# Kernel tuning notes

Hardware: AMD Instinct MI355X
Metric: run time of the kernel (lower is better)

The kernel has to match this reference:

```python
import jax, jax.numpy as jnp
import numpy as np

B, S, D = 2, 2048, 1024
H, HD = 16, 64          # num_heads, head_dim = dim_feedforward // num_heads
ROPE_BASE = 10000.0


def _apply_rope(t):
    # t: [b, h, s, hd] -> RoPE applied over last dim, positions = token index
    b, h, s, hd = t.shape
    theta = 1.0 / (ROPE_BASE ** (jnp.arange(0, hd, 2, dtype=jnp.float32) / hd))  # [hd/2]
    ang = jnp.arange(s, dtype=jnp.float32)[:, None] * theta[None, :]             # [s, hd/2]
    cos, sin = jnp.cos(ang), jnp.sin(ang)
    tr = t.reshape(b, h, s, hd // 2, 2)
    t0, t1 = tr[..., 0], tr[..., 1]
    o0 = t0 * cos - t1 * sin
    o1 = t1 * cos + t0 * sin
    return jnp.stack([o0, o1], axis=-1).reshape(b, h, s, hd)


def setup_inputs() -> dict:
    key = jax.random.key(0)
    ks = jax.random.split(key, 8)
    x = jax.random.normal(ks[0], (B, S, D), dtype=jnp.float32)
    wq = jax.random.normal(ks[1], (D, H * HD), dtype=jnp.float32) * 0.02
    wk = jax.random.normal(ks[2], (D, H * HD), dtype=jnp.float32) * 0.02
    wv = jax.random.normal(ks[3], (D, H * HD), dtype=jnp.float32) * 0.02
    bq = jax.random.normal(ks[4], (H * HD,), dtype=jnp.float32) * 0.02
    bk = jax.random.normal(ks[5], (H * HD,), dtype=jnp.float32) * 0.02
    bv = jax.random.normal(ks[6], (H * HD,), dtype=jnp.float32) * 0.02
    # trailing padding per batch; valid_len large enough that every causal+history
    # window contains at least one unpadded key (valid_len > S - max_history)
    valid_len = jax.random.randint(ks[7], (B,), S - 256, S + 1)
    key_padding_mask = (jnp.arange(S)[None, :] >= valid_len[:, None]).astype(jnp.int32)
    return {"x": x, "wq": wq, "bq": bq, "wk": wk, "bk": bk, "wv": wv, "bv": bv,
            "key_padding_mask": key_padding_mask, "max_history_len": 512}


def reference(x, wq, bq, wk, bk, wv, bv, key_padding_mask, max_history_len):
    b, s, d = x.shape
    scale = HD ** (-0.5)
    q = (x @ wq + bq).reshape(b, s, H, HD).transpose(0, 2, 1, 3)  # [b,h,s,hd]
    k = (x @ wk + bk).reshape(b, s, H, HD).transpose(0, 2, 1, 3)
    v = (x @ wv + bv).reshape(b, s, H, HD).transpose(0, 2, 1, 3)
    q = _apply_rope(q)
    k = _apply_rope(k)
    scores = jnp.einsum('bhqd,bhkd->bhqk', q, k) * scale          # [b,h,s,s]
    i = jnp.arange(s)[:, None]
    j = jnp.arange(s)[None, :]
    band = (j <= i) & ((i - j) <= (max_history_len - 1))          # causal + history
    allowed = band[None, None, :, :] & (key_padding_mask == 0)[:, None, None, :]
    scores = jnp.where(allowed, scores, -jnp.inf)
    attn = jax.nn.softmax(scores, axis=-1)
    out = jnp.einsum('bhqk,bhkd->bhqd', attn, v)                  # [b,h,s,hd]
    return out.transpose(0, 2, 1, 3).reshape(b, s, H * HD)
```

## Files before the change

kernel.cpp:

```cpp
#include <hip/hip_runtime.h>
#include <hip/hip_bf16.h>
#include <stdint.h>


typedef __attribute__((ext_vector_type(8))) short bf16x8;
typedef __attribute__((ext_vector_type(4))) short bf16x4;
typedef __attribute__((ext_vector_type(4))) float f32x4;

#define DEV __device__ __forceinline__

DEV ushort f2b(float f) {
  union { float f; uint32_t u; } v; v.f = f;
  uint32_t r = v.u + 0x7FFFu + ((v.u >> 16) & 1u);
  return (ushort)(r >> 16);
}
DEV float b2f(ushort u) {
  union { uint32_t u; float f; } v; v.u = ((uint32_t)u) << 16;
  return v.f;
}
DEV uint cvt_pk_bf16(float lo, float hi) {
  uint r;
  asm("v_cvt_pk_bf16_f32 %0, %1, %2" : "=v"(r) : "v"(lo), "v"(hi));
  return r;
}
DEV float fast_exp2(float x) {
#if __has_builtin(__builtin_amdgcn_exp2f)
  return __builtin_amdgcn_exp2f(x);
#else
  return exp2f(x);
#endif
}

DEV void gload_lds16(const void* g, void* l) {
  __builtin_amdgcn_global_load_lds((const __attribute__((address_space(1))) void*)g,
                                   (__attribute__((address_space(3))) void*)l,
                                   16, 0, 0);
}

__global__ __launch_bounds__(256) void prep_kernel(
    const float* __restrict__ x, ushort* __restrict__ xb,
    const float* __restrict__ wq, const float* __restrict__ wk,
    const float* __restrict__ wv, ushort* __restrict__ wt,
    float2* __restrict__ tab) {
  int bid = blockIdx.x, tid = threadIdx.x;
  if (bid < 4096) {
    int t = bid * 256 + tid;
    float4 v = ((const float4*)x)[t];
    bf16x4 o;
    o[0] = (short)f2b(v.x); o[1] = (short)f2b(v.y);
    o[2] = (short)f2b(v.z); o[3] = (short)f2b(v.w);
    *(bf16x4*)&xb[(size_t)t * 4] = o;
  } else if (bid < 4352) {
    int t = (bid - 4096) * 256 + tid;
    int i = t & 31, s = t >> 5;
    float theta = powf(10000.0f, -(float)i / 32.0f);
    float ang = (float)s * theta;
    tab[t] = make_float2(cosf(ang), sinf(ang));
  } else {
    __shared__ float tile[32][33];
    int rem = bid - 4352;
    int which = rem >> 10, t2 = rem & 1023;
    int n0 = (t2 & 31) * 32, k0 = (t2 >> 5) * 32;
    const float* w = which == 0 ? wq : (which == 1 ? wk : wv);
    int r = tid >> 3, c4 = (tid & 7) * 4;
    float4 v = *(const float4*)&w[(size_t)(k0 + r) * 1024 + n0 + c4];
    tile[r][c4] = v.x; tile[r][c4 + 1] = v.y;
    tile[r][c4 + 2] = v.z; tile[r][c4 + 3] = v.w;
    __syncthreads();
    bf16x4 o;
#pragma unroll
    for (int i = 0; i < 4; ++i) o[i] = (short)f2b(tile[c4 + i][r]);
    *(bf16x4*)&wt[((size_t)(which * 1024 + n0 + r)) * 1024 + k0 + c4] = o;
  }
}

__global__ __launch_bounds__(512, 2) void qkv_gemm_kernel(
    const ushort* __restrict__ A, const ushort* __restrict__ Bt,
    const float* __restrict__ bq, const float* __restrict__ bk,
    const float* __restrict__ bv, const float2* __restrict__ tab,
    ushort* __restrict__ qb, ushort* __restrict__ kb, ushort* __restrict__ vt) {
  const int K = 1024;
  __shared__ alignas(16) ushort sA[2][256 * 64];
  __shared__ alignas(16) ushort sB[2][192 * 64];

  int tid = threadIdx.x;
  int lane = tid & 63;
  int lhi = lane >> 4, llo = lane & 15;
  int wid = tid >> 6;
  int wr = wid >> 2, wc = wid & 3;

  int id = blockIdx.x;
  int wg = (id & 7) * 32 + (id >> 3);
  int bm = wg >> 4, bn = wg & 15;

  const ushort* Abase = A + (size_t)bm * 256 * K;
  const ushort* Bbase = Bt + (size_t)bn * 192 * K;

  f32x4 acc[8][3];
#pragma unroll
  for (int i = 0; i < 8; ++i)
#pragma unroll
    for (int j = 0; j < 3; ++j) acc[i][j] = (f32x4){0.f, 0.f, 0.f, 0.f};

  auto stage = [&](int kt, int bb) {
    int k0 = kt * 64;
#pragma unroll
    for (int c = 0; c < 4; ++c) {
      int idx = c * 512 + tid;
      int row = idx >> 3, gslot = (idx & 7) ^ (row & 7);
      gload_lds16(Abase + (size_t)row * K + k0 + gslot * 8, &sA[bb][(idx & ~63) * 8]);
    }
#pragma unroll
    for (int c = 0; c < 3; ++c) {
      int idx = c * 512 + tid;
      int row = idx >> 3, gslot = (idx & 7) ^ (row & 7);
      gload_lds16(Bbase + (size_t)row * K + k0 + gslot * 8, &sB[bb][(idx & ~63) * 8]);
    }
  };

  bf16x8 bfr[3][2], af0[4][2], af1[4][2];

  auto readG0 = [&](const ushort* pA, const ushort* pB) {
#pragma unroll
    for (int nf = 0; nf < 3; ++nf) {
      int r = wc * 48 + nf * 16 + llo;
#pragma unroll
      for (int ks = 0; ks < 2; ++ks)
        bfr[nf][ks] = *(const bf16x8*)&pB[r * 64 + (((ks * 4 + lhi) ^ (r & 7)) * 8)];
    }
#pragma unroll
    for (int mf = 0; mf < 4; ++mf) {
      int r = wr * 128 + mf * 16 + llo;
#pragma unroll
      for (int ks = 0; ks < 2; ++ks)
        af0[mf][ks] = *(const bf16x8*)&pA[r * 64 + (((ks * 4 + lhi) ^ (r & 7)) * 8)];
    }
  };
  auto readG1 = [&](const ushort* pA) {
#pragma unroll
    for (int mf = 0; mf < 4; ++mf) {
      int r = wr * 128 + (4 + mf) * 16 + llo;
#pragma unroll
      for (int ks = 0; ks < 2; ++ks)
        af1[mf][ks] = *(const bf16x8*)&pA[r * 64 + (((ks * 4 + lhi) ^ (r & 7)) * 8)];
    }
  };

  stage(0, 0); stage(1, 1);
  asm volatile("s_waitcnt vmcnt(7)" ::: "memory");
  __builtin_amdgcn_sched_barrier(0);
  __builtin_amdgcn_s_barrier();
  __builtin_amdgcn_sched_barrier(0);
  readG0(sA[0], sB[0]);

  for (int kt = 0; kt < 16; ++kt) {
    int buf = kt & 1;
    readG1(sA[buf]);
    asm volatile("s_waitcnt lgkmcnt(8)" ::: "memory");
    __builtin_amdgcn_sched_barrier(0);
    __builtin_amdgcn_s_setprio(1);
#pragma unroll
    for (int mf = 0; mf < 4; ++mf)
#pragma unroll
      for (int nf = 0; nf < 3; ++nf)
#pragma unroll
        for (int ks = 0; ks < 2; ++ks)
          acc[mf][nf] = __builtin_amdgcn_mfma_f32_16x16x32_bf16(bfr[nf][ks], af0[mf][ks], acc[mf][nf], 0, 0, 0);
    __builtin_amdgcn_s_setprio(0);
    asm volatile("s_waitcnt lgkmcnt(0)" ::: "memory");
    __builtin_amdgcn_sched_barrier(0);
    __builtin_amdgcn_s_setprio(1);
#pragma unroll
    for (int mf = 0; mf < 4; ++mf)
#pragma unroll
      for (int nf = 0; nf < 3; ++nf)
#pragma unroll
        for (int ks = 0; ks < 2; ++ks)
          acc[4 + mf][nf] = __builtin_amdgcn_mfma_f32_16x16x32_bf16(bfr[nf][ks], af1[mf][ks], acc[4 + mf][nf], 0, 0, 0);
    __builtin_amdgcn_s_setprio(0);
    __builtin_amdgcn_sched_barrier(0);
    __builtin_amdgcn_s_barrier();
    __builtin_amdgcn_sched_barrier(0);
    if (kt + 2 < 16) stage(kt + 2, buf);
    if (kt + 1 < 16) {
      if (kt + 2 < 16) asm volatile("s_waitcnt vmcnt(7)" ::: "memory");
      else             asm volatile("s_waitcnt vmcnt(0)" ::: "memory");
      __builtin_amdgcn_sched_barrier(0);
      __builtin_amdgcn_s_barrier();
      __builtin_amdgcn_sched_barrier(0);
      readG0(sA[buf ^ 1], sB[buf ^ 1]);
    }
  }

  const float SCL = 0.18033688011112042f;
#pragma unroll
  for (int mf = 0; mf < 8; ++mf) {
    int m = bm * 256 + wr * 128 + mf * 16 + llo;
    int s = m & 2047, bidx = m >> 11;
#pragma unroll
    for (int nf = 0; nf < 3; ++nf) {
      int nbase = bn * 192 + wc * 48 + nf * 16;
      int n0 = nbase + lhi * 4;
      f32x4 a = acc[mf][nf];
      if (nbase < 1024) {
        float4 cs = *(const float4*)&tab[s * 32 + ((n0 & 63) >> 1)];
        float4 bb = *(const float4*)&bq[n0];
        float t0 = a[0] + bb.x, t1 = a[1] + bb.y;
        float t2 = a[2] + bb.z, t3 = a[3] + bb.w;
        uint2 ov;
        ov.x = cvt_pk_bf16((t0 * cs.x - t1 * cs.y) * SCL, (t1 * cs.x + t0 * cs.y) * SCL);
        ov.y = cvt_pk_bf16((t2 * cs.z - t3 * cs.w) * SCL, (t3 * cs.z + t2 * cs.w) * SCL);
        int h = n0 >> 6;
        *(uint2*)&qb[((size_t)(bidx * 16 + h) * 2048 + s) * 64 + (n0 & 63)] = ov;
      } else if (nbase < 2048) {
        float4 cs = *(const float4*)&tab[s * 32 + ((n0 & 63) >> 1)];
        float4 bb = *(const float4*)&bk[n0 - 1024];
        float t0 = a[0] + bb.x, t1 = a[1] + bb.y;
        float t2 = a[2] + bb.z, t3 = a[3] + bb.w;
        uint2 ov;
        ov.x = cvt_pk_bf16(t0 * cs.x - t1 * cs.y, t1 * cs.x + t0 * cs.y);
        ov.y = cvt_pk_bf16(t2 * cs.z - t3 * cs.w, t3 * cs.z + t2 * cs.w);
        int h = (n0 >> 6) & 15;
        *(uint2*)&kb[((size_t)(bidx * 16 + h) * 2048 + s) * 64 + (n0 & 63)] = ov;
      } else {
        float4 bb = *(const float4*)&bv[n0 - 2048];
        int hd_g = n0 - 2048;
        int h = hd_g >> 6, hd = hd_g & 63;
        size_t vb = ((size_t)(bidx * 16 + h) * 64 + hd) * 2048 + s;
        vt[vb]        = f2b(a[0] + bb.x);
        vt[vb + 2048] = f2b(a[1] + bb.y);
        vt[vb + 4096] = f2b(a[2] + bb.z);
        vt[vb + 6144] = f2b(a[3] + bb.w);
      }
    }
  }
}

__global__ __launch_bounds__(512) void attn_kernel(
    const ushort* __restrict__ qb, const ushort* __restrict__ kb,
    const ushort* __restrict__ vt, const int* __restrict__ kmask,
    const int* __restrict__ whist, float* __restrict__ out) {
  __shared__ alignas(16) ushort sK[128 * 64];
  __shared__ alignas(16) ushort sV[64 * 136];
  __shared__ alignas(16) uint   sPd[8][16 * 68];

  int tid = threadIdx.x;
  int lane = tid & 63, wid = tid >> 6;
  int lhi = lane >> 4, llo = lane & 15;

  int id = blockIdx.x;
  int xcd = id & 7, sub = id >> 3;
  int bh = xcd * 4 + (sub >> 4);
  int qtile = sub & 15;
  int b = bh >> 4;
  int q0 = qtile * 128;
  int qw0 = q0 + wid * 16;
  int W = *whist;

  const ushort* qptr = qb + (size_t)bh * 2048 * 64;
  const ushort* kptr = kb + (size_t)bh * 2048 * 64;
  const ushort* vptr = vt + (size_t)bh * 64 * 2048;
  const int* mrow = kmask + b * 2048;

  bf16x8 qf0, qf1;
  {
    size_t base = (size_t)(qw0 + llo) * 64 + lhi * 8;
    qf0 = *(const bf16x8*)&qptr[base];
    qf1 = *(const bf16x8*)&qptr[base + 32];
  }

  float l_ = 0.f;
  f32x4 o[4];
#pragma unroll
  for (int nf = 0; nf < 4; ++nf) o[nf] = (f32x4){0.f, 0.f, 0.f, 0.f};

  int lo = q0 - (W - 1); if (lo < 0) lo = 0;
  int jt0 = lo & ~127;
  int nt = ((q0 + 128) - jt0) >> 7;

  bf16x8 kreg[2], vreg[2];
  int mreg0, mreg1;
  int krow = tid >> 2, kslot2 = (tid & 3) * 2;
  int vrow = tid >> 3, vslot2 = (tid & 7) * 2;

  auto load_tile = [&](int jt) {
    kreg[0] = *(const bf16x8*)&kptr[(size_t)(jt + krow) * 64 + kslot2 * 8];
    kreg[1] = *(const bf16x8*)&kptr[(size_t)(jt + krow) * 64 + (kslot2 + 1) * 8];
    vreg[0] = *(const bf16x8*)&vptr[(size_t)vrow * 2048 + jt + vslot2 * 8];
    vreg[1] = *(const bf16x8*)&vptr[(size_t)vrow * 2048 + jt + (vslot2 + 1) * 8];
    mreg0 = mrow[jt + lane];
    mreg1 = mrow[jt + 64 + lane];
  };

  load_tile(jt0);
  for (int it = 0; it < nt; ++it) {
    int jt = jt0 + it * 128;
    __syncthreads();
    *(bf16x8*)&sK[krow * 64 + ((kslot2 ^ (krow & 7)) * 8)] = kreg[0];
    *(bf16x8*)&sK[krow * 64 + (((kslot2 + 1) ^ (krow & 7)) * 8)] = kreg[1];
    *(bf16x8*)&sV[vrow * 136 + vslot2 * 8] = vreg[0];
    *(bf16x8*)&sV[vrow * 136 + (vslot2 + 1) * 8] = vreg[1];
    unsigned long long pm0 = __ballot(mreg0 != 0);
    unsigned long long pm1 = __ballot(mreg1 != 0);
    if (it + 1 < nt) load_tile(jt + 128);
    __syncthreads();

    bool active = (jt <= qw0 + 15) && (jt + 127 >= qw0 - W + 1);
    if (active) {
      f32x4 sc[8];
#pragma unroll
      for (int kb8 = 0; kb8 < 8; ++kb8) sc[kb8] = (f32x4){0.f, 0.f, 0.f, 0.f};
      __builtin_amdgcn_s_setprio(1);
#pragma unroll
      for (int ks = 0; ks < 2; ++ks) {
        bf16x8 qq = ks ? qf1 : qf0;
#pragma unroll
        for (int kb8 = 0; kb8 < 8; ++kb8) {
          int r = kb8 * 16 + llo;
          bf16x8 kf = *(const bf16x8*)&sK[r * 64 + (((ks * 4 + lhi) ^ (r & 7)) * 8)];
          sc[kb8] = __builtin_amdgcn_mfma_f32_16x16x32_bf16(kf, qq, sc[kb8], 0, 0, 0);
        }
      }
      __builtin_amdgcn_s_setprio(0);

      bool fastp = (jt + 127 <= qw0) && (jt >= qw0 + 16 - W) &&
                   (pm0 == 0ull) && (pm1 == 0ull);
      if (!fastp) {
        int qi = qw0 + llo;
#pragma unroll
        for (int kb8 = 0; kb8 < 8; ++kb8) {
          uint nib = (uint)((kb8 < 4 ? pm0 : pm1) >> ((kb8 & 3) * 16 + lhi * 4)) & 0xFu;
#pragma unroll
          for (int j = 0; j < 4; ++j) {
            int key = jt + kb8 * 16 + lhi * 4 + j;
            bool k_ok = (key <= qi) && (qi - key < W) && !((nib >> j) & 1u);
            sc[kb8][j] = k_ok ? sc[kb8][j] : -1e30f;
          }
        }
      }

#pragma unroll
      for (int kb8 = 0; kb8 < 8; ++kb8)
#pragma unroll
        for (int j = 0; j < 4; ++j) sc[kb8][j] = fast_exp2(sc[kb8][j]);

      uint* prow = &sPd[wid][llo * 68];
#pragma unroll
      for (int kb8 = 0; kb8 < 8; ++kb8) {
        uint2 d;
        d.x = cvt_pk_bf16(sc[kb8][0], sc[kb8][1]);
        d.y = cvt_pk_bf16(sc[kb8][2], sc[kb8][3]);
        *(uint2*)&prow[kb8 * 8 + lhi * 2] = d;
      }

      float sm[8];
#pragma unroll
      for (int kb8 = 0; kb8 < 8; ++kb8)
        sm[kb8] = (sc[kb8][0] + sc[kb8][1]) + (sc[kb8][2] + sc[kb8][3]);
      l_ += ((sm[0] + sm[1]) + (sm[2] + sm[3])) + ((sm[4] + sm[5]) + (sm[6] + sm[7]));

      bf16x8 pf[4];
#pragma unroll
      for (int ksb = 0; ksb < 4; ++ksb)
        pf[ksb] = *(const bf16x8*)&sPd[wid][llo * 68 + ksb * 16 + lhi * 4];

      __builtin_amdgcn_s_setprio(1);
#pragma unroll
      for (int nf = 0; nf < 4; ++nf) {
#pragma unroll
        for (int ksb = 0; ksb < 4; ++ksb) {
          bf16x8 vf = *(const bf16x8*)&sV[(nf * 16 + llo) * 136 + ksb * 32 + lhi * 8];
          o[nf] = __builtin_amdgcn_mfma_f32_16x16x32_bf16(vf, pf[ksb], o[nf], 0, 0, 0);
        }
      }
      __builtin_amdgcn_s_setprio(0);
    }
  }

  l_ += __shfl_xor(l_, 16);
  l_ += __shfl_xor(l_, 32);
  float inv = 1.f / l_;
  int qi = qw0 + llo;
  size_t obase = ((size_t)b * 2048 + qi) * 1024 + (bh & 15) * 64 + lhi * 4;
#pragma unroll
  for (int nf = 0; nf < 4; ++nf) {
    float4 st = make_float4(o[nf][0] * inv, o[nf][1] * inv, o[nf][2] * inv, o[nf][3] * inv);
    *(float4*)&out[obase + nf * 16] = st;
  }
}

extern "C" void kernel_launch(void* const* d_in, const int* in_sizes, int n_in,
                              void* d_out, int out_size, void* d_ws, size_t ws_size,
                              hipStream_t stream) {
  const float* x  = (const float*)d_in[0];
  const float* wq = (const float*)d_in[1];
  const float* bq = (const float*)d_in[2];
  const float* wk = (const float*)d_in[3];
  const float* bk = (const float*)d_in[4];
  const float* wv = (const float*)d_in[5];
  const float* bv = (const float*)d_in[6];
  const int* kmask = (const int*)d_in[7];
  const int* whist = (const int*)d_in[8];
  float* out = (float*)d_out;

  char* ws = (char*)d_ws;
  ushort* xb  = (ushort*)(ws);
  ushort* wt  = (ushort*)(ws + (8ull  << 20));
  ushort* qb  = (ushort*)(ws + (14ull << 20));
  ushort* kb  = (ushort*)(ws + (22ull << 20));
  ushort* vt  = (ushort*)(ws + (30ull << 20));
  float2* tab = (float2*)(ws + (38ull << 20));

  prep_kernel<<<7424, 256, 0, stream>>>(x, xb, wq, wk, wv, wt, tab);
  qkv_gemm_kernel<<<256, 512, 0, stream>>>(xb, wt, bq, bk, bv, tab, qb, kb, vt);
  attn_kernel<<<512, 512, 0, stream>>>(qb, kb, vt, kmask, whist, out);
}
```

Measured before the change: 70.99 us.

## Replace direct global-to-LDS loads with register-staged loads in QKV GEMM

The GEMM's staging changes from global_load_lds (direct to LDS) to ordinary global loads into two register buffers, followed by swizzled ds_write stores. The prefetch runs three tiles ahead: two held in registers and one in LDS. One barrier per iteration is removed, and the loop is unrolled by two so the register buffers alternate. This costs extra VGPRs (14 uint4) and explicit LDS write instructions, which may hurt occupancy or issue rate.

```diff
diff --git a/kernel.cpp b/kernel.cpp
--- a/kernel.cpp
+++ b/kernel.cpp
@@ -29,12 +29,6 @@
 #else
   return exp2f(x);
 #endif
-}
-
-DEV void gload_lds16(const void* g, void* l) {
-  __builtin_amdgcn_global_load_lds((const __attribute__((address_space(1))) void*)g,
-                                   (__attribute__((address_space(3))) void*)l,
-                                   16, 0, 0);
 }
 
 __global__ __launch_bounds__(256) void prep_kernel(
@@ -102,19 +96,29 @@
 #pragma unroll
     for (int j = 0; j < 3; ++j) acc[i][j] = (f32x4){0.f, 0.f, 0.f, 0.f};
 
-  auto stage = [&](int kt, int bb) {
+  auto gload = [&](int kt, uint4 (&R)[7]) {
     int k0 = kt * 64;
 #pragma unroll
     for (int c = 0; c < 4; ++c) {
-      int idx = c * 512 + tid;
-      int row = idx >> 3, gslot = (idx & 7) ^ (row & 7);
-      gload_lds16(Abase + (size_t)row * K + k0 + gslot * 8, &sA[bb][(idx & ~63) * 8]);
+      int idx = c * 512 + tid, row = idx >> 3, slot = idx & 7;
+      R[c] = *(const uint4*)&Abase[(size_t)row * K + k0 + slot * 8];
     }
 #pragma unroll
     for (int c = 0; c < 3; ++c) {
-      int idx = c * 512 + tid;
-      int row = idx >> 3, gslot = (idx & 7) ^ (row & 7);
-      gload_lds16(Bbase + (size_t)row * K + k0 + gslot * 8, &sB[bb][(idx & ~63) * 8]);
+      int idx = c * 512 + tid, row = idx >> 3, slot = idx & 7;
+      R[4 + c] = *(const uint4*)&Bbase[(size_t)row * K + k0 + slot * 8];
+    }
+  };
+  auto dswrite = [&](int bb, uint4 (&R)[7]) {
+#pragma unroll
+    for (int c = 0; c < 4; ++c) {
+      int idx = c * 512 + tid, row = idx >> 3, slot = idx & 7;
+      *(uint4*)&sA[bb][row * 64 + ((slot ^ (row & 7)) * 8)] = R[c];
+    }
+#pragma unroll
+    for (int c = 0; c < 3; ++c) {
+      int idx = c * 512 + tid, row = idx >> 3, slot = idx & 7;
+      *(uint4*)&sB[bb][row * 64 + ((slot ^ (row & 7)) * 8)] = R[4 + c];
     }
   };
 
@@ -146,16 +150,23 @@
     }
   };
 
-  stage(0, 0); stage(1, 1);
-  asm volatile("s_waitcnt vmcnt(7)" ::: "memory");
+  uint4 R0[7], R1[7];
+
+  gload(0, R0);
+  asm volatile("s_waitcnt vmcnt(0)" ::: "memory");
+  __builtin_amdgcn_sched_barrier(0);
+  dswrite(0, R0);
+  gload(1, R0);
+  gload(2, R1);
+  asm volatile("s_waitcnt lgkmcnt(0)" ::: "memory");
   __builtin_amdgcn_sched_barrier(0);
   __builtin_amdgcn_s_barrier();
   __builtin_amdgcn_sched_barrier(0);
   readG0(sA[0], sB[0]);
 
-  for (int kt = 0; kt < 16; ++kt) {
+  auto tile_body = [&](int kt, uint4 (&Rcur)[7], uint4 (&Rnext)[7]) {
     int buf = kt & 1;
-    readG1(sA[buf]);
+    readG1(buf ? sA[1] : sA[0]);
     asm volatile("s_waitcnt lgkmcnt(8)" ::: "memory");
     __builtin_amdgcn_sched_barrier(0);
     __builtin_amdgcn_s_setprio(1);
@@ -179,17 +190,24 @@
           acc[4 + mf][nf] = __builtin_amdgcn_mfma_f32_16x16x32_bf16(bfr[nf][ks], af1[mf][ks], acc[4 + mf][nf], 0, 0, 0);
     __builtin_amdgcn_s_setprio(0);
     __builtin_amdgcn_sched_barrier(0);
-    __builtin_amdgcn_s_barrier();
-    __builtin_amdgcn_sched_barrier(0);
-    if (kt + 2 < 16) stage(kt + 2, buf);
+
     if (kt + 1 < 16) {
-      if (kt + 2 < 16) asm volatile("s_waitcnt vmcnt(7)" ::: "memory");
-      else             asm volatile("s_waitcnt vmcnt(0)" ::: "memory");
+      if (kt < 14) asm volatile("s_waitcnt vmcnt(7)" ::: "memory");
+      else         asm volatile("s_waitcnt vmcnt(0)" ::: "memory");
+      __builtin_amdgcn_sched_barrier(0);
+      dswrite((kt + 1) & 1, Rcur);
+      if (kt + 3 < 16) gload(kt + 3, Rcur);
+      asm volatile("s_waitcnt lgkmcnt(0)" ::: "memory");
       __builtin_amdgcn_sched_barrier(0);
       __builtin_amdgcn_s_barrier();
       __builtin_amdgcn_sched_barrier(0);
-      readG0(sA[buf ^ 1], sB[buf ^ 1]);
-    }
+      readG0((kt + 1) & 1 ? sA[1] : sA[0], (kt + 1) & 1 ? sB[1] : sB[0]);
+    }
+  };
+
+  for (int kt = 0; kt < 16; kt += 2) {
+    tile_body(kt, R0, R1);
+    tile_body(kt + 1, R1, R0);
   }
 
   const float SCL = 0.18033688011112042f;
```

After: 114.8 us. 61.7% more time.
